# Kernel optimization log

Measured on AMD Instinct MI355X. Metric: run time of the kernel, lower is better.

## Reference

```python
import jax, jax.numpy as jnp
import numpy as np

N_NODES = 50000
N_EDGES = 800000
IN_DIM = 128
HEADS = 8
HEAD_DIM = 16


def setup_inputs() -> dict:
    key = jax.random.key(0)
    ks = jax.random.split(key, 9)
    s = 1.0 / np.sqrt(IN_DIM)
    return {
        "h": jax.random.normal(ks[0], (N_NODES, IN_DIM), dtype=jnp.float32),
        "src": jax.random.randint(ks[1], (N_EDGES,), 0, N_NODES, dtype=jnp.int32),
        "dst": jax.random.randint(ks[2], (N_EDGES,), 0, N_NODES, dtype=jnp.int32),
        "WQ": jax.random.normal(ks[3], (IN_DIM, HEADS * HEAD_DIM), dtype=jnp.float32) * s,
        "bQ": jnp.zeros((HEADS * HEAD_DIM,), dtype=jnp.float32),
        "WK": jax.random.normal(ks[4], (IN_DIM, HEADS * HEAD_DIM), dtype=jnp.float32) * s,
        "bK": jnp.zeros((HEADS * HEAD_DIM,), dtype=jnp.float32),
        "WV": jax.random.normal(ks[5], (IN_DIM, HEADS * HEAD_DIM), dtype=jnp.float32) * s,
        "bV": jnp.zeros((HEADS * HEAD_DIM,), dtype=jnp.float32),
    }


def reference(h, src, dst, WQ, bQ, WK, bK, WV, bV):
    N = h.shape[0]
    sqrt_d = jnp.float32(np.sqrt(HEAD_DIM))
    # node projections, viewed as [N, H, D]
    Q = (h @ WQ + bQ).reshape(N, HEADS, HEAD_DIM)
    K = (h @ WK + bK).reshape(N, HEADS, HEAD_DIM)
    V = (h @ WV + bV).reshape(N, HEADS, HEAD_DIM)
    # edge scores: (K_src . Q_dst) per head, scaled exp with clamp [-5, 5]
    score = jnp.sum(K[src] * Q[dst], axis=-1, keepdims=True)  # [E, H, 1]
    score = jnp.exp(jnp.clip(score / sqrt_d, -5.0, 5.0))
    # segment-softmax denominator z and weighted V sum wV, both scattered to dst
    z = jax.ops.segment_sum(score, dst, num_segments=N)            # [N, H, 1]
    wV = jax.ops.segment_sum(V[src] * score, dst, num_segments=N)  # [N, H, D]
    # possible_empty: divide only where z > 0 (wV is 0 there anyway)
    head_out = jnp.where(z > 0, wV / jnp.where(z > 0, z, 1.0), wV)
    return head_out
```

## Files before the change

### kernel.cpp

```cpp
#include <hip/hip_runtime.h>
#include <math.h>

#define DIM 128
#define N_HEADS 8
#define HD 16
#define CAP 64


typedef __attribute__((ext_vector_type(8))) short bf16x8;
typedef __attribute__((ext_vector_type(4))) float f32x4;

__device__ __forceinline__ unsigned bf16pack2(float a, float b) {
    unsigned ua = __builtin_bit_cast(unsigned, a);
    unsigned ub = __builtin_bit_cast(unsigned, b);
    ua = (ua + 0x7FFFu + ((ua >> 16) & 1u)) >> 16;
    ub = (ub + 0x7FFFu + ((ub >> 16) & 1u)) >> 16;
    return ua | (ub << 16);
}
__device__ __forceinline__ float bf16lo(unsigned p) {
    return __builtin_bit_cast(float, p << 16);
}
__device__ __forceinline__ float bf16hi(unsigned p) {
    return __builtin_bit_cast(float, p & 0xFFFF0000u);
}

__global__ __launch_bounds__(256)
void init_kernel(const float* __restrict__ WQ, const float* __restrict__ bQ,
                 const float* __restrict__ WK, const float* __restrict__ bK,
                 const float* __restrict__ WV, const float* __restrict__ bV,
                 unsigned short* __restrict__ WT, float* __restrict__ bias384,
                 int* __restrict__ cnt, int NB, int N)
{
    if ((int)blockIdx.x < NB) {
        int i = blockIdx.x * 256 + threadIdx.x;
        if (i < N) cnt[i] = 0;
    } else {
        int idx = ((int)blockIdx.x - NB) * 256 + threadIdx.x;
        int c = idx >> 7, k = idx & 127;
        const float* W; const float* b; int col = c & 127;
        if (c < 128)      { W = WQ; b = bQ; }
        else if (c < 256) { W = WK; b = bK; }
        else              { W = WV; b = bV; }
        float v = W[k * DIM + col];
        WT[(size_t)c * DIM + k] = (unsigned short)(bf16pack2(v, 0.0f) & 0xFFFFu);
        if (k == 0) bias384[c] = b[col];
    }
}

__global__ __launch_bounds__(256)
void append_kernel(const int* __restrict__ src, const int* __restrict__ dst,
                   int* __restrict__ cnt, unsigned short* __restrict__ srcsF, int E)
{
    int t = (blockIdx.x * 256 + threadIdx.x) * 4;
    if (t + 3 < E) {
        int4 d4 = *(const int4*)(dst + t);
        int4 s4 = *(const int4*)(src + t);
        int sl0 = atomicAdd(&cnt[d4.x], 1);
        int sl1 = atomicAdd(&cnt[d4.y], 1);
        int sl2 = atomicAdd(&cnt[d4.z], 1);
        int sl3 = atomicAdd(&cnt[d4.w], 1);
        if (sl0 < CAP) srcsF[(size_t)d4.x * CAP + sl0] = (unsigned short)s4.x;
        if (sl1 < CAP) srcsF[(size_t)d4.y * CAP + sl1] = (unsigned short)s4.y;
        if (sl2 < CAP) srcsF[(size_t)d4.z * CAP + sl2] = (unsigned short)s4.z;
        if (sl3 < CAP) srcsF[(size_t)d4.w * CAP + sl3] = (unsigned short)s4.w;
    } else {
        for (int e = t; e < E; ++e) {
            int d    = dst[e];
            int slot = atomicAdd(&cnt[d], 1);
            if (slot < CAP) srcsF[(size_t)d * CAP + slot] = (unsigned short)src[e];
        }
    }
}

__global__ __launch_bounds__(256)
void qkv_mfma_kernel(const float* __restrict__ h,
                     const unsigned short* __restrict__ WT,
                     const float* __restrict__ bias384,
                     unsigned* __restrict__ Qd, unsigned* __restrict__ KVd,
                     int N)
{
    __shared__ unsigned short hs[64 * 136];
    const int tid = threadIdx.x;
    const int n0  = blockIdx.x * 64;

    #pragma unroll
    for (int i = 0; i < 4; ++i) {
        int lin  = i * 256 + tid;
        int node = lin >> 4;
        int k0   = (lin & 15) * 8;
        int gn   = n0 + node;
        float4 a0, a1;
        if (gn < N) {
            a0 = *(const float4*)(h + (size_t)gn * DIM + k0);
            a1 = *(const float4*)(h + (size_t)gn * DIM + k0 + 4);
        } else {
            a0 = make_float4(0.f, 0.f, 0.f, 0.f);
            a1 = a0;
        }
        uint4 p = make_uint4(bf16pack2(a0.x, a0.y), bf16pack2(a0.z, a0.w),
                             bf16pack2(a1.x, a1.y), bf16pack2(a1.z, a1.w));
        *(uint4*)(hs + node * 136 + k0) = p;
    }
    __syncthreads();

    const int wave   = tid >> 6;
    const int l      = tid & 63;
    const int lane16 = l & 15;
    const int quad   = l >> 4;
    const int wc0    = wave * 96;

    f32x4 acc[6][4];
    #pragma unroll
    for (int ct = 0; ct < 6; ++ct) {
        float4 bv = *(const float4*)(bias384 + wc0 + ct * 16 + quad * 4);
        #pragma unroll
        for (int rt = 0; rt < 4; ++rt)
            acc[ct][rt] = (f32x4){bv.x, bv.y, bv.z, bv.w};
    }

    #pragma unroll
    for (int ks = 0; ks < 4; ++ks) {
        bf16x8 a[6], b[4];
        #pragma unroll
        for (int ct = 0; ct < 6; ++ct)
            a[ct] = *(const bf16x8*)(WT + (size_t)(wc0 + ct * 16 + lane16) * DIM
                                         + ks * 32 + quad * 8);
        #pragma unroll
        for (int rt = 0; rt < 4; ++rt)
            b[rt] = *(const bf16x8*)(hs + (rt * 16 + lane16) * 136 + ks * 32 + quad * 8);
        #pragma unroll
        for (int ct = 0; ct < 6; ++ct)
            #pragma unroll
            for (int rt = 0; rt < 4; ++rt)
                acc[ct][rt] = __builtin_amdgcn_mfma_f32_16x16x32_bf16(
                    a[ct], b[rt], acc[ct][rt], 0, 0, 0);
    }

    #pragma unroll
    for (int ct = 0; ct < 6; ++ct) {
        const int col = wc0 + ct * 16 + quad * 4;
        #pragma unroll
        for (int rt = 0; rt < 4; ++rt) {
            int gn = n0 + rt * 16 + lane16;
            if (gn >= N) continue;
            f32x4 v = acc[ct][rt];
            uint2 pr = make_uint2(bf16pack2(v[0], v[1]), bf16pack2(v[2], v[3]));
            if (col < 128) {
                *(uint2*)(Qd + (size_t)gn * 64 + (col >> 1)) = pr;
            } else if (col < 256) {
                int c = col - 128;
                *(uint2*)(KVd + (size_t)gn * 128 + ((c >> 3) * 8) + ((c & 4) >> 1)) = pr;
            } else {
                int c = col - 256;
                *(uint2*)(KVd + (size_t)gn * 128 + ((c >> 3) * 8) + 4 + ((c & 4) >> 1)) = pr;
            }
        }
    }
}

__device__ __forceinline__ void agg_chunk16(
    const unsigned* __restrict__ KVd, int eg, int deg, int slot, int c,
    const int* raw,
    float q0, float q1, float q2, float q3,
    float q4, float q5, float q6, float q7,
    float acc[8], float& zs)
{
    bool val[4];
    const uint4* p[4];
    #pragma unroll
    for (int j = 0; j < 4; ++j) {
        int ee = eg + j * 4 + slot;
        val[j] = ee < deg;
        int s  = val[j] ? raw[j] : 0;
        p[j]   = (const uint4*)(KVd + (size_t)s * 128 + c * 8);
    }
    uint4 K[4], V[4];
    #pragma unroll
    for (int j = 0; j < 4; ++j) { K[j] = p[j][0]; V[j] = p[j][1]; }

    float d[4];
    #pragma unroll
    for (int j = 0; j < 4; ++j)
        d[j] = bf16lo(K[j].x) * q0 + bf16hi(K[j].x) * q1
             + bf16lo(K[j].y) * q2 + bf16hi(K[j].y) * q3
             + bf16lo(K[j].z) * q4 + bf16hi(K[j].z) * q5
             + bf16lo(K[j].w) * q6 + bf16hi(K[j].w) * q7;
    #pragma unroll
    for (int j = 0; j < 4; ++j) d[j] += __shfl_xor(d[j], 1);

    #pragma unroll
    for (int j = 0; j < 4; ++j) {
        float pc = fminf(fmaxf(d[j] * 0.25f, -5.0f), 5.0f);
        float w  = val[j] ? __expf(pc) : 0.0f;
        zs += w;
        acc[0] += w * bf16lo(V[j].x); acc[1] += w * bf16hi(V[j].x);
        acc[2] += w * bf16lo(V[j].y); acc[3] += w * bf16hi(V[j].y);
        acc[4] += w * bf16lo(V[j].z); acc[5] += w * bf16hi(V[j].z);
        acc[6] += w * bf16lo(V[j].w); acc[7] += w * bf16hi(V[j].w);
    }
}

__global__ __launch_bounds__(256, 4)
void aggregate_kernel(const int* __restrict__ cnt,
                      const unsigned short* __restrict__ srcsF,
                      const unsigned* __restrict__ Qd, const unsigned* __restrict__ KVd,
                      float* __restrict__ out, int N)
{
    const int l      = threadIdx.x & 63;
    const int slot   = l >> 4;
    const int c      = l & 15;
    const int stride = gridDim.x * 4;

    int node = blockIdx.x * 4 + (threadIdx.x >> 6);
    if (node >= N) return;

    int   deg = cnt[node];
    uint4 qd  = *(const uint4*)(Qd + (size_t)node * 64 + c * 4);
    int   pb[8];
    {
        const unsigned short* b = srcsF + (size_t)node * CAP;
        #pragma unroll
        for (int j = 0; j < 8; ++j)
            pb[j] = b[((j >> 2) << 4) + ((j & 3) << 2) + slot];
    }

    for (;;) {
        const int  nnode   = node + stride;
        const bool hasNext = nnode < N;

        int ndeg = 0; uint4 nqd = make_uint4(0u, 0u, 0u, 0u); int npb[8];
        #pragma unroll
        for (int j = 0; j < 8; ++j) npb[j] = 0;
        if (hasNext) {
            ndeg = cnt[nnode];
            nqd  = *(const uint4*)(Qd + (size_t)nnode * 64 + c * 4);
            const unsigned short* b = srcsF + (size_t)nnode * CAP;
            #pragma unroll
            for (int j = 0; j < 8; ++j)
                npb[j] = b[((j >> 2) << 4) + ((j & 3) << 2) + slot];
        }

        int degc = deg > CAP ? CAP : deg;
        const float q0 = bf16lo(qd.x), q1 = bf16hi(qd.x);
        const float q2 = bf16lo(qd.y), q3 = bf16hi(qd.y);
        const float q4 = bf16lo(qd.z), q5 = bf16hi(qd.z);
        const float q6 = bf16lo(qd.w), q7 = bf16hi(qd.w);

        float acc[8] = {0.f, 0.f, 0.f, 0.f, 0.f, 0.f, 0.f, 0.f};
        float zs = 0.f;

        if (degc > 0)
            agg_chunk16(KVd, 0, degc, slot, c, pb,
                        q0, q1, q2, q3, q4, q5, q6, q7, acc, zs);
        if (degc > 16)
            agg_chunk16(KVd, 16, degc, slot, c, pb + 4,
                        q0, q1, q2, q3, q4, q5, q6, q7, acc, zs);
        for (int eg = 32; eg < degc; eg += 16) {
            int raw[4];
            const unsigned short* b = srcsF + (size_t)node * CAP;
            #pragma unroll
            for (int j = 0; j < 4; ++j) {
                int ee = eg + j * 4 + slot;
                raw[j] = b[ee < degc ? ee : 0];
            }
            agg_chunk16(KVd, eg, degc, slot, c, raw,
                        q0, q1, q2, q3, q4, q5, q6, q7, acc, zs);
        }

        #pragma unroll
        for (int j = 0; j < 8; ++j) {
            acc[j] += __shfl_xor(acc[j], 16);
            acc[j] += __shfl_xor(acc[j], 32);
        }
        zs += __shfl_xor(zs, 16);
        zs += __shfl_xor(zs, 32);

        if (slot == 0) {
            float inv = (zs > 0.0f) ? (1.0f / zs) : 0.0f;
            *(float4*)(out + (size_t)node * DIM + c * 8) =
                make_float4(acc[0] * inv, acc[1] * inv, acc[2] * inv, acc[3] * inv);
            *(float4*)(out + (size_t)node * DIM + c * 8 + 4) =
                make_float4(acc[4] * inv, acc[5] * inv, acc[6] * inv, acc[7] * inv);
        }

        if (!hasNext) break;
        node = nnode; deg = ndeg; qd = nqd;
        #pragma unroll
        for (int j = 0; j < 8; ++j) pb[j] = npb[j];
    }
}

extern "C" void kernel_launch(void* const* d_in, const int* in_sizes, int n_in,
                              void* d_out, int out_size, void* d_ws, size_t ws_size,
                              hipStream_t stream) {
    const float* h   = (const float*)d_in[0];
    const int*   src = (const int*)  d_in[1];
    const int*   dst = (const int*)  d_in[2];
    const float* WQ  = (const float*)d_in[3];
    const float* bQ  = (const float*)d_in[4];
    const float* WK  = (const float*)d_in[5];
    const float* bK  = (const float*)d_in[6];
    const float* WV  = (const float*)d_in[7];
    const float* bV  = (const float*)d_in[8];
    float* out = (float*)d_out;

    const int N  = in_sizes[0] / DIM;
    const int E  = in_sizes[1];
    const int NB = (N + 255) / 256;
    const int EB = (E / 4 + 255) / 256;
    const int QB = (N + 63) / 64;
    const int nConv = (384 * DIM) / 256;

    char* w = (char*)d_ws;
    unsigned*       Qd      = (unsigned*)w;        w += (size_t)N * 64  * sizeof(unsigned);
    unsigned*       KVd     = (unsigned*)w;        w += (size_t)N * 128 * sizeof(unsigned);
    unsigned short* WT      = (unsigned short*)w;  w += (size_t)384 * DIM * sizeof(unsigned short);
    float*          bias384 = (float*)w;           w += 384 * sizeof(float);
    int*            cnt     = (int*)w;             w += (size_t)N * sizeof(int);
    unsigned short* srcsF   = (unsigned short*)w;

    init_kernel<<<NB + nConv, 256, 0, stream>>>(WQ, bQ, WK, bK, WV, bV,
                                                WT, bias384, cnt, NB, N);
    append_kernel<<<EB, 256, 0, stream>>>(src, dst, cnt, srcsF, E);
    qkv_mfma_kernel<<<QB, 256, 0, stream>>>(h, WT, bias384, Qd, KVd, N);
    aggregate_kernel<<<2048, 256, 0, stream>>>(cnt, srcsF, Qd, KVd, out, N);
}
```

Before: 230.1 us.

## Fuse edge append and QKV projection into one launch, drop weight pre-conversion

Merges the edge-append kernel and the QKV MFMA projection into one grid, with block ranges split by index, so the atomic-heavy bucketing can overlap with the GEMM. The separate init kernel that transposed the weights to bf16 is removed. The GEMM now reads fp32 weights directly, with strided per-column loads converted to bf16 on the fly, and cnt is cleared with hipMemsetAsync. This cuts launches and a dependency step, but adds uncoalesced strided weight reads in every GEMM block.

```diff
diff --git a/kernel.cpp b/kernel.cpp
--- a/kernel.cpp
+++ b/kernel.cpp
@@ -6,9 +6,10 @@
 #define HD 16
 #define CAP 64
 
-
 typedef __attribute__((ext_vector_type(8))) short bf16x8;
 typedef __attribute__((ext_vector_type(4))) float f32x4;
+typedef __attribute__((ext_vector_type(4))) unsigned ui32x4;
+
 
 __device__ __forceinline__ unsigned bf16pack2(float a, float b) {
     unsigned ua = __builtin_bit_cast(unsigned, a);
@@ -25,63 +26,43 @@
 }
 
 __global__ __launch_bounds__(256)
-void init_kernel(const float* __restrict__ WQ, const float* __restrict__ bQ,
-                 const float* __restrict__ WK, const float* __restrict__ bK,
-                 const float* __restrict__ WV, const float* __restrict__ bV,
-                 unsigned short* __restrict__ WT, float* __restrict__ bias384,
-                 int* __restrict__ cnt, int NB, int N)
-{
-    if ((int)blockIdx.x < NB) {
-        int i = blockIdx.x * 256 + threadIdx.x;
-        if (i < N) cnt[i] = 0;
-    } else {
-        int idx = ((int)blockIdx.x - NB) * 256 + threadIdx.x;
-        int c = idx >> 7, k = idx & 127;
-        const float* W; const float* b; int col = c & 127;
-        if (c < 128)      { W = WQ; b = bQ; }
-        else if (c < 256) { W = WK; b = bK; }
-        else              { W = WV; b = bV; }
-        float v = W[k * DIM + col];
-        WT[(size_t)c * DIM + k] = (unsigned short)(bf16pack2(v, 0.0f) & 0xFFFFu);
-        if (k == 0) bias384[c] = b[col];
-    }
-}
-
-__global__ __launch_bounds__(256)
-void append_kernel(const int* __restrict__ src, const int* __restrict__ dst,
-                   int* __restrict__ cnt, unsigned short* __restrict__ srcsF, int E)
-{
-    int t = (blockIdx.x * 256 + threadIdx.x) * 4;
-    if (t + 3 < E) {
-        int4 d4 = *(const int4*)(dst + t);
-        int4 s4 = *(const int4*)(src + t);
-        int sl0 = atomicAdd(&cnt[d4.x], 1);
-        int sl1 = atomicAdd(&cnt[d4.y], 1);
-        int sl2 = atomicAdd(&cnt[d4.z], 1);
-        int sl3 = atomicAdd(&cnt[d4.w], 1);
-        if (sl0 < CAP) srcsF[(size_t)d4.x * CAP + sl0] = (unsigned short)s4.x;
-        if (sl1 < CAP) srcsF[(size_t)d4.y * CAP + sl1] = (unsigned short)s4.y;
-        if (sl2 < CAP) srcsF[(size_t)d4.z * CAP + sl2] = (unsigned short)s4.z;
-        if (sl3 < CAP) srcsF[(size_t)d4.w * CAP + sl3] = (unsigned short)s4.w;
-    } else {
-        for (int e = t; e < E; ++e) {
-            int d    = dst[e];
-            int slot = atomicAdd(&cnt[d], 1);
-            if (slot < CAP) srcsF[(size_t)d * CAP + slot] = (unsigned short)src[e];
-        }
-    }
-}
-
-__global__ __launch_bounds__(256)
-void qkv_mfma_kernel(const float* __restrict__ h,
-                     const unsigned short* __restrict__ WT,
-                     const float* __restrict__ bias384,
-                     unsigned* __restrict__ Qd, unsigned* __restrict__ KVd,
-                     int N)
+void append_qkv_kernel(const int* __restrict__ src, const int* __restrict__ dst,
+                       int* __restrict__ cnt, unsigned short* __restrict__ srcsF,
+                       int E, int AB,
+                       const float* __restrict__ h,
+                       const float* __restrict__ WQ, const float* __restrict__ bQ,
+                       const float* __restrict__ WK, const float* __restrict__ bK,
+                       const float* __restrict__ WV, const float* __restrict__ bV,
+                       unsigned* __restrict__ Qd, unsigned* __restrict__ KVd,
+                       int N)
 {
     __shared__ unsigned short hs[64 * 136];
+
+    if ((int)blockIdx.x < AB) {
+        int t = (blockIdx.x * 256 + threadIdx.x) * 4;
+        if (t + 3 < E) {
+            int4 d4 = *(const int4*)(dst + t);
+            int4 s4 = *(const int4*)(src + t);
+            int sl0 = atomicAdd(&cnt[d4.x], 1);
+            int sl1 = atomicAdd(&cnt[d4.y], 1);
+            int sl2 = atomicAdd(&cnt[d4.z], 1);
+            int sl3 = atomicAdd(&cnt[d4.w], 1);
+            if (sl0 < CAP) srcsF[(size_t)d4.x * CAP + sl0] = (unsigned short)s4.x;
+            if (sl1 < CAP) srcsF[(size_t)d4.y * CAP + sl1] = (unsigned short)s4.y;
+            if (sl2 < CAP) srcsF[(size_t)d4.z * CAP + sl2] = (unsigned short)s4.z;
+            if (sl3 < CAP) srcsF[(size_t)d4.w * CAP + sl3] = (unsigned short)s4.w;
+        } else {
+            for (int e = t; e < E; ++e) {
+                int d    = dst[e];
+                int slot = atomicAdd(&cnt[d], 1);
+                if (slot < CAP) srcsF[(size_t)d * CAP + slot] = (unsigned short)src[e];
+            }
+        }
+        return;
+    }
+
     const int tid = threadIdx.x;
-    const int n0  = blockIdx.x * 64;
+    const int n0  = ((int)blockIdx.x - AB) * 64;
 
     #pragma unroll
     for (int i = 0; i < 4; ++i) {
@@ -109,10 +90,19 @@
     const int quad   = l >> 4;
     const int wc0    = wave * 96;
 
+    const float* Wm[6]; const float* bm[6]; int cb[6];
+    #pragma unroll
+    for (int ct = 0; ct < 6; ++ct) {
+        int col0 = wc0 + ct * 16;
+        if (col0 < 128)      { Wm[ct] = WQ; bm[ct] = bQ; cb[ct] = col0; }
+        else if (col0 < 256) { Wm[ct] = WK; bm[ct] = bK; cb[ct] = col0 - 128; }
+        else                 { Wm[ct] = WV; bm[ct] = bV; cb[ct] = col0 - 256; }
+    }
+
     f32x4 acc[6][4];
     #pragma unroll
     for (int ct = 0; ct < 6; ++ct) {
-        float4 bv = *(const float4*)(bias384 + wc0 + ct * 16 + quad * 4);
+        float4 bv = *(const float4*)(bm[ct] + cb[ct] + quad * 4);
         #pragma unroll
         for (int rt = 0; rt < 4; ++rt)
             acc[ct][rt] = (f32x4){bv.x, bv.y, bv.z, bv.w};
@@ -120,11 +110,17 @@
 
     #pragma unroll
     for (int ks = 0; ks < 4; ++ks) {
+        const int kb = ks * 32 + quad * 8;
         bf16x8 a[6], b[4];
         #pragma unroll
-        for (int ct = 0; ct < 6; ++ct)
-            a[ct] = *(const bf16x8*)(WT + (size_t)(wc0 + ct * 16 + lane16) * DIM
-                                         + ks * 32 + quad * 8);
+        for (int ct = 0; ct < 6; ++ct) {
+            const float* wp = Wm[ct] + (size_t)kb * DIM + cb[ct] + lane16;
+            float w0 = wp[0 * DIM], w1 = wp[1 * DIM], w2 = wp[2 * DIM], w3 = wp[3 * DIM];
+            float w4 = wp[4 * DIM], w5 = wp[5 * DIM], w6 = wp[6 * DIM], w7 = wp[7 * DIM];
+            ui32x4 pk = { bf16pack2(w0, w1), bf16pack2(w2, w3),
+                          bf16pack2(w4, w5), bf16pack2(w6, w7) };
+            a[ct] = __builtin_bit_cast(bf16x8, pk);
+        }
         #pragma unroll
         for (int rt = 0; rt < 4; ++rt)
             b[rt] = *(const bf16x8*)(hs + (rt * 16 + lane16) * 136 + ks * 32 + quad * 8);
@@ -306,22 +302,18 @@
 
     const int N  = in_sizes[0] / DIM;
     const int E  = in_sizes[1];
-    const int NB = (N + 255) / 256;
-    const int EB = (E / 4 + 255) / 256;
+    const int AB = (E / 4 + 255) / 256;
     const int QB = (N + 63) / 64;
-    const int nConv = (384 * DIM) / 256;
 
     char* w = (char*)d_ws;
-    unsigned*       Qd      = (unsigned*)w;        w += (size_t)N * 64  * sizeof(unsigned);
-    unsigned*       KVd     = (unsigned*)w;        w += (size_t)N * 128 * sizeof(unsigned);
-    unsigned short* WT      = (unsigned short*)w;  w += (size_t)384 * DIM * sizeof(unsigned short);
-    float*          bias384 = (float*)w;           w += 384 * sizeof(float);
-    int*            cnt     = (int*)w;             w += (size_t)N * sizeof(int);
-    unsigned short* srcsF   = (unsigned short*)w;
-
-    init_kernel<<<NB + nConv, 256, 0, stream>>>(WQ, bQ, WK, bK, WV, bV,
-                                                WT, bias384, cnt, NB, N);
-    append_kernel<<<EB, 256, 0, stream>>>(src, dst, cnt, srcsF, E);
-    qkv_mfma_kernel<<<QB, 256, 0, stream>>>(h, WT, bias384, Qd, KVd, N);
+    unsigned*       Qd    = (unsigned*)w;       w += (size_t)N * 64  * sizeof(unsigned);
+    unsigned*       KVd   = (unsigned*)w;       w += (size_t)N * 128 * sizeof(unsigned);
+    int*            cnt   = (int*)w;            w += (size_t)N * sizeof(int);
+    unsigned short* srcsF = (unsigned short*)w;
+
+    hipMemsetAsync(cnt, 0, (size_t)N * sizeof(int), stream);
+    append_qkv_kernel<<<AB + QB, 256, 0, stream>>>(src, dst, cnt, srcsF, E, AB,
+                                                   h, WQ, bQ, WK, bK, WV, bV,
+                                                   Qd, KVd, N);
     aggregate_kernel<<<2048, 256, 0, stream>>>(cnt, srcsF, Qd, KVd, out, N);
 }
```

New measurement: 215.9 us. -6.2%, faster.
